# Optimization experiments

Hardware: AMD Instinct MI355X
Metric: run time of the kernel (lower is better)

## Reference

```python
import jax, jax.numpy as jnp
import numpy as np
from jax import lax

NPOINT, RADIUS, NSAMPLE, K_KEY = 64, 1.0, 32, 64

def conv1d(x, W, b):
    # 1x1 Conv1d: x [B,Cin,N], W [Cout,Cin], b [Cout] -> [B,Cout,N]
    return jnp.einsum('bcn,dc->bdn', x, W) + b[None, :, None]

def farthest_point_sample(xyz, npoint):
    # xyz [B,N,3] -> idx [B,npoint]
    B, N, _ = xyz.shape
    dist0 = jnp.full((B, N), 1e10, dtype=xyz.dtype)
    far0 = jnp.zeros((B,), dtype=jnp.int32)
    def body(carry, _):
        dist, far = carry
        centroid = jnp.take_along_axis(xyz, far[:, None, None].astype(jnp.int32), axis=1)  # [B,1,3]
        d = jnp.sum((xyz - centroid) ** 2, -1)
        dist = jnp.minimum(dist, d)
        nxt = jnp.argmax(dist, -1).astype(jnp.int32)
        return (dist, nxt), far
    _, idxs = lax.scan(body, (dist0, far0), None, length=npoint)
    return idxs.T  # [B,npoint]

def ball_query(radius, nsample, xyz, new_xyz):
    # xyz [B,N,3], new_xyz [B,S,3] -> group_idx [B,S,nsample]
    N = xyz.shape[1]
    sqr = jnp.sum((new_xyz[:, :, None, :] - xyz[:, None, :, :]) ** 2, -1)  # [B,S,N]
    gidx = jnp.where(sqr > radius ** 2, N, jnp.arange(N, dtype=jnp.int32)[None, None, :])
    gidx = jnp.sort(gidx, axis=-1)[..., :nsample]
    first = gidx[..., :1]
    gidx = jnp.where(gidx == N, first, gidx)
    return gidx

def sample_and_group(npoint, radius, nsample, xyz, points):
    # xyz [B,N,3], points [B,N,D]
    B = xyz.shape[0]
    fps_idx = farthest_point_sample(xyz, npoint)                     # [B,S]
    bidx = jnp.arange(B)[:, None]
    new_xyz = xyz[bidx, fps_idx]                                     # [B,S,3]
    gidx = ball_query(radius, nsample, xyz, new_xyz)                 # [B,S,ns]
    bidx2 = jnp.arange(B)[:, None, None]
    grouped_xyz = xyz[bidx2, gidx]                                   # [B,S,ns,3]
    grouped_xyz_norm = grouped_xyz - new_xyz[:, :, None, :]
    grouped_points = points[bidx2, gidx]                             # [B,S,ns,D]
    new_points = jnp.concatenate([grouped_xyz_norm, grouped_points], axis=-1)
    return new_xyz, new_points

def setup_inputs() -> dict:
    key = jax.random.key(0)
    ks = jax.random.split(key, 12)
    B, C, N = 8, 6, 65536
    def w(k, co, ci):
        return jax.random.normal(k, (co, ci), jnp.float32) * (1.0 / np.sqrt(ci))
    return {
        'src_pts': jax.random.normal(ks[0], (B, C, N), jnp.float32),
        'tgt_pts': jax.random.normal(ks[1], (B, C, N), jnp.float32),
        'W1': w(ks[2], 32, 6),  'b1': jnp.zeros((32,), jnp.float32),
        'W2': w(ks[3], 64, 32), 'b2': jnp.zeros((64,), jnp.float32),
        'Wa': w(ks[4], 16, 64), 'ba': jnp.zeros((16,), jnp.float32),
        'Wb': w(ks[5], 8, 16),  'bb': jnp.zeros((8,), jnp.float32),
        'Wc': w(ks[6], 1, 8),   'bc': jnp.zeros((1,), jnp.float32),
    }

def reference(src_pts, tgt_pts, W1, b1, W2, b2, Wa, ba, Wb, bb, Wc, bc):
    # feat_extraction_layer: 1x1 conv stack over points -> deep per-point features
    h = jax.nn.relu(conv1d(src_pts, W1, b1))            # [B,32,N]
    deep_feat_pts = jax.nn.relu(conv1d(h, W2, b2))      # [B,64,N]
    # weighting_layer: per-point saliency weight + top-k keypoint indices (1-D, batch-0 idiom)
    w = jax.nn.relu(conv1d(deep_feat_pts, Wa, ba))
    w = jax.nn.relu(conv1d(w, Wb, bb))
    w = jax.nn.softplus(conv1d(w, Wc, bc))              # [B,1,N]
    _, keypts_idx = lax.top_k(w[0, 0], K_KEY)           # [K]
    # irregular keypoint gather (shared index across batch, as in src_pts[:, :, idx])
    src_keypts = src_pts[:, :, keypts_idx].transpose(0, 2, 1)   # [B,K,C]
    # ball-query sample_and_group on keypoints (computed then discarded, as in original)
    _gxyz, _gpts = sample_and_group(NPOINT, RADIUS, NSAMPLE, src_keypts[:, :, :3], src_keypts[:, :, 3:])
    return src_keypts
```

## Files before the change

kernel.cpp:

```cpp
#include <hip/hip_runtime.h>
#include <stdint.h>

#define N_PTS 65536
#define NB1 32768
#define NB2 4096
#define CAND_CAP 4096
#define FCAP 1024
typedef unsigned long long u64;


__global__ __launch_bounds__(256) void zero_kernel(uint4* __restrict__ z, int n4)
{
    const int i = blockIdx.x * 256 + threadIdx.x;
    const uint4 zz = {0u, 0u, 0u, 0u};
    if (i < n4) z[i] = zz;
}

__global__ __launch_bounds__(128, 1) void score_kernel(
    const float* __restrict__ src,
    const float* __restrict__ W1, const float* __restrict__ b1,
    const float* __restrict__ W2, const float* __restrict__ b2,
    const float* __restrict__ Wa, const float* __restrict__ ba,
    const float* __restrict__ Wb, const float* __restrict__ bb,
    const float* __restrict__ Wc, const float* __restrict__ bc,
    float* __restrict__ scores, unsigned* __restrict__ hist1)
{
    __shared__ unsigned histL[NB1];
    __shared__ __align__(16) float sW1[32 * 8];
    __shared__ __align__(16) float sW2[64 * 32];
    __shared__ __align__(16) float sWaT[64 * 16];
    __shared__ __align__(16) float sWb[8 * 16];
    __shared__ float sb2[64], sba[16], sbb[8], sWc[8], sbc1[1];
    const int t = threadIdx.x;

    {
        uint4* h4 = (uint4*)histL;
        const uint4 zz = {0u, 0u, 0u, 0u};
        #pragma unroll
        for (int i = 0; i < 64; i++) h4[t + 128 * i] = zz;
    }
    for (int i = t; i < 256; i += 128) {
        const int j = i >> 3, c = i & 7;
        sW1[i] = (c < 6) ? W1[j * 6 + c] : ((c == 6) ? b1[j] : 0.f);
    }
    for (int i = t; i < 2048; i += 128) sW2[i] = W2[i];
    for (int i = t; i < 1024; i += 128) {
        const int j = i >> 4, q = i & 15;
        sWaT[i] = Wa[q * 64 + j];
    }
    if (t < 128) sWb[t] = Wb[t];
    if (t < 64)  sb2[t] = b2[t];
    if (t < 16)  sba[t] = ba[t];
    if (t < 8)   { sbb[t] = bb[t]; sWc[t] = Wc[t]; }
    if (t == 0)  sbc1[0] = bc[0];
    __syncthreads();

    const int base = blockIdx.x * 256;
    const int p[2] = { base + t, base + 128 + t };

    float x[2][6];
    #pragma unroll
    for (int c = 0; c < 6; c++) {
        x[0][c] = src[c * N_PTS + p[0]];
        x[1][c] = src[c * N_PTS + p[1]];
    }

    float h1[2][32];
    #pragma unroll
    for (int j = 0; j < 32; j++) {
        const float4 wA = *(const float4*)&sW1[j * 8];
        const float4 wB = *(const float4*)&sW1[j * 8 + 4];
        #pragma unroll
        for (int P = 0; P < 2; P++) {
            float a = wB.z;
            a = fmaf(wA.x, x[P][0], a); a = fmaf(wA.y, x[P][1], a);
            a = fmaf(wA.z, x[P][2], a); a = fmaf(wA.w, x[P][3], a);
            a = fmaf(wB.x, x[P][4], a); a = fmaf(wB.y, x[P][5], a);
            h1[P][j] = fmaxf(a, 0.f);
        }
    }

    float h3[2][16];
    #pragma unroll
    for (int q = 0; q < 16; q++) { h3[0][q] = sba[q]; h3[1][q] = sba[q]; }

    #pragma unroll 1
    for (int jb = 0; jb < 32; jb++) {
        const int j0 = 2 * jb, j1 = j0 + 1;
        const float4* r0 = (const float4*)&sW2[j0 * 32];
        const float4* r1 = (const float4*)&sW2[j1 * 32];
        const float4* wa0 = (const float4*)&sWaT[j0 * 16];
        const float4* wa1 = (const float4*)&sWaT[j1 * 16];
        float4 u[8], v[8], q0[4], q1[4];
        #pragma unroll
        for (int i = 0; i < 8; i++) u[i] = r0[i];
        #pragma unroll
        for (int i = 0; i < 8; i++) v[i] = r1[i];
        #pragma unroll
        for (int i = 0; i < 4; i++) q0[i] = wa0[i];
        #pragma unroll
        for (int i = 0; i < 4; i++) q1[i] = wa1[i];
        const float bj0 = sb2[j0], bj1 = sb2[j1];

        #pragma unroll
        for (int P = 0; P < 2; P++) {
            float a0 = 0.f, a1 = 0.f, a2 = 0.f, a3 = 0.f;
            float c0 = 0.f, c1 = 0.f, c2 = 0.f, c3 = 0.f;
            #pragma unroll
            for (int i4 = 0; i4 < 8; i4++) {
                const float h0 = h1[P][4 * i4 + 0], hh1 = h1[P][4 * i4 + 1];
                const float h2 = h1[P][4 * i4 + 2], hh3 = h1[P][4 * i4 + 3];
                a0 = fmaf(u[i4].x, h0, a0); a1 = fmaf(u[i4].y, hh1, a1);
                a2 = fmaf(u[i4].z, h2, a2); a3 = fmaf(u[i4].w, hh3, a3);
                c0 = fmaf(v[i4].x, h0, c0); c1 = fmaf(v[i4].y, hh1, c1);
                c2 = fmaf(v[i4].z, h2, c2); c3 = fmaf(v[i4].w, hh3, c3);
            }
            const float v0 = fmaxf((a0 + a1) + (a2 + a3) + bj0, 0.f);
            const float v1 = fmaxf((c0 + c1) + (c2 + c3) + bj1, 0.f);
            #pragma unroll
            for (int q4 = 0; q4 < 4; q4++) {
                float t0 = h3[P][4 * q4 + 0], t1 = h3[P][4 * q4 + 1];
                float t2 = h3[P][4 * q4 + 2], t3 = h3[P][4 * q4 + 3];
                t0 = fmaf(q0[q4].x, v0, t0); t1 = fmaf(q0[q4].y, v0, t1);
                t2 = fmaf(q0[q4].z, v0, t2); t3 = fmaf(q0[q4].w, v0, t3);
                t0 = fmaf(q1[q4].x, v1, t0); t1 = fmaf(q1[q4].y, v1, t1);
                t2 = fmaf(q1[q4].z, v1, t2); t3 = fmaf(q1[q4].w, v1, t3);
                h3[P][4 * q4 + 0] = t0; h3[P][4 * q4 + 1] = t1;
                h3[P][4 * q4 + 2] = t2; h3[P][4 * q4 + 3] = t3;
            }
        }
    }
    #pragma unroll
    for (int q = 0; q < 16; q++) {
        h3[0][q] = fmaxf(h3[0][q], 0.f);
        h3[1][q] = fmaxf(h3[1][q], 0.f);
    }

    float z[2] = { sbc1[0], sbc1[0] };
    #pragma unroll
    for (int j = 0; j < 8; j++) {
        const float4* wbr = (const float4*)&sWb[j * 16];
        const float4 w0 = wbr[0], w1 = wbr[1], w2 = wbr[2], w3 = wbr[3];
        const float bj = sbb[j], wc = sWc[j];
        #pragma unroll
        for (int P = 0; P < 2; P++) {
            float s0 = bj, s1 = 0.f, s2 = 0.f, s3 = 0.f;
            s0 = fmaf(w0.x, h3[P][0],  s0); s1 = fmaf(w0.y, h3[P][1],  s1);
            s2 = fmaf(w0.z, h3[P][2],  s2); s3 = fmaf(w0.w, h3[P][3],  s3);
            s0 = fmaf(w1.x, h3[P][4],  s0); s1 = fmaf(w1.y, h3[P][5],  s1);
            s2 = fmaf(w1.z, h3[P][6],  s2); s3 = fmaf(w1.w, h3[P][7],  s3);
            s0 = fmaf(w2.x, h3[P][8],  s0); s1 = fmaf(w2.y, h3[P][9],  s1);
            s2 = fmaf(w2.z, h3[P][10], s2); s3 = fmaf(w2.w, h3[P][11], s3);
            s0 = fmaf(w3.x, h3[P][12], s0); s1 = fmaf(w3.y, h3[P][13], s1);
            s2 = fmaf(w3.z, h3[P][14], s2); s3 = fmaf(w3.w, h3[P][15], s3);
            z[P] = fmaf(wc, fmaxf((s0 + s1) + (s2 + s3), 0.f), z[P]);
        }
    }

    #pragma unroll
    for (int P = 0; P < 2; P++) {
        const float sp = fmaxf(z[P], 0.f) + log1pf(expf(-fabsf(z[P])));
        scores[p[P]] = sp;
        atomicAdd(&histL[__float_as_uint(sp) >> 16], 1u);
    }
    __syncthreads();

    {
        const uint4* h4 = (const uint4*)histL;
        for (int i = t; i < NB1 / 4; i += 128) {
            const uint4 v = h4[i];
            if (v.x) atomicAdd(&hist1[4 * i + 0], v.x);
            if (v.y) atomicAdd(&hist1[4 * i + 1], v.y);
            if (v.z) atomicAdd(&hist1[4 * i + 2], v.z);
            if (v.w) atomicAdd(&hist1[4 * i + 3], v.w);
        }
    }
}

__global__ __launch_bounds__(256) void refine_kernel(
    const unsigned* __restrict__ hist1, const float* __restrict__ scores,
    unsigned* __restrict__ hist2, int* __restrict__ meta,
    u64* __restrict__ cand)
{
    __shared__ unsigned csum[256];
    __shared__ unsigned bsum[128];
    __shared__ int sh_c, sh_B;
    __shared__ unsigned sh_tail;
    const int t = threadIdx.x;

    {
        unsigned s = 0;
        const uint4* h4 = (const uint4*)(hist1 + t * 128);
        #pragma unroll
        for (int i = 0; i < 32; i++) {
            const uint4 v = h4[i];
            s += v.x + v.y + v.z + v.w;
        }
        csum[t] = s;
    }
    __syncthreads();
    for (int d = 1; d < 256; d <<= 1) {
        const unsigned v = (t + d < 256) ? csum[t + d] : 0u;
        __syncthreads();
        csum[t] += v;
        __syncthreads();
    }
    {
        const unsigned here = csum[t];
        const unsigned nxt = (t + 1 < 256) ? csum[t + 1] : 0u;
        if (here >= 64u && nxt < 64u) sh_c = t;
    }
    __syncthreads();
    const int cstar = sh_c;
    if (t < 128) bsum[t] = hist1[cstar * 128 + t];
    __syncthreads();
    {
        const unsigned ctail = (cstar + 1 < 256) ? csum[cstar + 1] : 0u;
        for (int d = 1; d < 128; d <<= 1) {
            unsigned v = 0u;
            if (t < 128 && t + d < 128) v = bsum[t + d];
            __syncthreads();
            if (t < 128) bsum[t] += v;
            __syncthreads();
        }
        if (t < 128) {
            const unsigned here = bsum[t] + ctail;
            const unsigned nxt = (t + 1 < 128) ? bsum[t + 1] + ctail : ctail;
            if (here >= 64u && nxt < 64u) { sh_B = cstar * 128 + t; sh_tail = nxt; }
        }
    }
    __syncthreads();
    const unsigned Bstar = (unsigned)sh_B;
    if (blockIdx.x == 0 && t == 0) { meta[0] = sh_B; meta[1] = (int)sh_tail; }

    const float4* s4 = (const float4*)scores;
    const int i = blockIdx.x * 256 + t;
    const float4 v = s4[i];
    const int n0 = 4 * i;
    #pragma unroll
    for (int k = 0; k < 4; k++) {
        const float sv = (k == 0) ? v.x : (k == 1) ? v.y : (k == 2) ? v.z : v.w;
        const unsigned b = __float_as_uint(sv);
        const unsigned hi = b >> 16;
        if (hi >= Bstar) {
            const int p = atomicAdd(&meta[2], 1);
            if (p < CAND_CAP) cand[p] = ((u64)b << 32) | (unsigned)~(n0 + k);
            if (hi == Bstar) atomicAdd(&hist2[(b & 0xFFFFu) >> 4], 1u);
        }
    }
}

__global__ __launch_bounds__(256) void final_kernel(
    const unsigned* __restrict__ hist2, const int* __restrict__ meta,
    const u64* __restrict__ cand, const float* __restrict__ src,
    float* __restrict__ out)
{
    __shared__ unsigned h2[NB2];
    __shared__ unsigned csum[256];
    __shared__ u64 keys[FCAP];
    __shared__ int idxs[64];
    __shared__ int sh_c, sh_T2, sh_cnt;
    const int t = threadIdx.x;
    const unsigned Bstar = (unsigned)meta[0];
    const unsigned tail1 = (unsigned)meta[1];

    {
        uint4* d = (uint4*)h2;
        const uint4* s = (const uint4*)hist2;
        #pragma unroll
        for (int i = 0; i < 4; i++) d[t + 256 * i] = s[t + 256 * i];
    }
    __syncthreads();

    {
        unsigned s = 0;
        #pragma unroll
        for (int i = 0; i < 16; i++) s += h2[t * 16 + i];
        csum[t] = s;
    }
    __syncthreads();
    for (int d = 1; d < 256; d <<= 1) {
        const unsigned v = (t + d < 256) ? csum[t + d] : 0u;
        __syncthreads();
        csum[t] += v;
        __syncthreads();
    }
    {
        const unsigned here = tail1 + csum[t];
        const unsigned nxt = tail1 + ((t + 1 < 256) ? csum[t + 1] : 0u);
        if (here >= 64u && nxt < 64u) sh_c = t;
    }
    __syncthreads();
    {
        const int c2 = sh_c;
        if (t == 0) {
            unsigned acc = tail1 + ((c2 + 1 < 256) ? csum[c2 + 1] : 0u);
            int T2 = c2 * 16;
            for (int b = c2 * 16 + 15; b >= c2 * 16; b--) {
                acc += h2[b];
                if (acc >= 64u) { T2 = b; break; }
            }
            sh_T2 = T2;
            sh_cnt = 0;
        }
    }
    __syncthreads();
    const unsigned T2 = (unsigned)sh_T2;

    int count = meta[2];
    if (count > CAND_CAP) count = CAND_CAP;
    for (int i = t; i < count; i += 256) {
        const u64 key = cand[i];
        const unsigned b = (unsigned)(key >> 32);
        const unsigned hi = b >> 16;
        if (hi > Bstar || ((b & 0xFFFFu) >> 4) >= T2) {
            const int p = atomicAdd(&sh_cnt, 1);
            if (p < FCAP) keys[p] = key;
        }
    }
    __syncthreads();

    int fcnt = sh_cnt;
    if (fcnt > FCAP) fcnt = FCAP;
    for (int i = t; i < fcnt; i += 256) {
        const u64 me = keys[i];
        int r = 0;
        for (int j = 0; j < fcnt; j++) r += (keys[j] > me);
        if (r < 64) idxs[r] = (int)~(unsigned)(me & 0xFFFFFFFFu);
    }
    __syncthreads();

    for (int e = t; e < 3072; e += 256) {
        const int b  = e / 384;
        const int rr = e % 384;
        const int kk = rr / 6;
        const int c  = rr % 6;
        out[e] = src[(b * 6 + c) * N_PTS + idxs[kk]];
    }
}

extern "C" void kernel_launch(void* const* d_in, const int* in_sizes, int n_in,
                              void* d_out, int out_size, void* d_ws, size_t ws_size,
                              hipStream_t stream)
{
    const float* src = (const float*)d_in[0];
    const float* W1 = (const float*)d_in[2];
    const float* b1 = (const float*)d_in[3];
    const float* W2 = (const float*)d_in[4];
    const float* b2 = (const float*)d_in[5];
    const float* Wa = (const float*)d_in[6];
    const float* ba = (const float*)d_in[7];
    const float* Wb = (const float*)d_in[8];
    const float* bb = (const float*)d_in[9];
    const float* Wc = (const float*)d_in[10];
    const float* bc = (const float*)d_in[11];

    char* ws = (char*)d_ws;
    float*    scores = (float*)ws;
    unsigned* hist1  = (unsigned*)(ws + 256 * 1024);
    unsigned* hist2  = (unsigned*)(ws + 384 * 1024);
    int*      meta   = (int*)(ws + 400 * 1024);
    u64*      cand   = (u64*)(ws + 408 * 1024);
    float*    out    = (float*)d_out;

    const int n4 = (NB1 + NB2 + 16) / 4;
    zero_kernel<<<(n4 + 255) / 256, 256, 0, stream>>>((uint4*)hist1, n4);
    score_kernel<<<256, 128, 0, stream>>>(src, W1, b1, W2, b2, Wa, ba,
                                          Wb, bb, Wc, bc, scores, hist1);
    refine_kernel<<<64, 256, 0, stream>>>(hist1, scores, hist2, meta, cand);
    final_kernel<<<1, 256, 0, stream>>>(hist2, meta, cand, src, out);
}
```

Baseline: 148.6 us.

## Fuse final selection into refine via last-block pattern and enlarge score blocks

The final single-block kernel is merged into refine_kernel: each block increments a completion counter after its candidate pass, and only the last-arriving block runs the final top-k selection and gather. This removes one kernel launch and its serialization gap. score_kernel also moves from 256 blocks of 128 threads to 64 blocks of 512 threads, so fewer blocks each zero and flush the 32K-bin shared histogram, cutting global atomic traffic. The cost is only 64 blocks on a large GPU for the MLP work, plus threadfence ordering and the counter in meta[3], which must be zeroed before each call.

```diff
diff --git a/kernel.cpp b/kernel.cpp
--- a/kernel.cpp
+++ b/kernel.cpp
@@ -16,7 +16,7 @@
     if (i < n4) z[i] = zz;
 }
 
-__global__ __launch_bounds__(128, 1) void score_kernel(
+__global__ __launch_bounds__(512, 1) void score_kernel(
     const float* __restrict__ src,
     const float* __restrict__ W1, const float* __restrict__ b1,
     const float* __restrict__ W2, const float* __restrict__ b2,
@@ -37,14 +37,14 @@
         uint4* h4 = (uint4*)histL;
         const uint4 zz = {0u, 0u, 0u, 0u};
         #pragma unroll
-        for (int i = 0; i < 64; i++) h4[t + 128 * i] = zz;
-    }
-    for (int i = t; i < 256; i += 128) {
-        const int j = i >> 3, c = i & 7;
-        sW1[i] = (c < 6) ? W1[j * 6 + c] : ((c == 6) ? b1[j] : 0.f);
-    }
-    for (int i = t; i < 2048; i += 128) sW2[i] = W2[i];
-    for (int i = t; i < 1024; i += 128) {
+        for (int i = 0; i < 16; i++) h4[t + 512 * i] = zz;
+    }
+    if (t < 256) {
+        const int j = t >> 3, c = t & 7;
+        sW1[t] = (c < 6) ? W1[j * 6 + c] : ((c == 6) ? b1[j] : 0.f);
+    }
+    for (int i = t; i < 2048; i += 512) sW2[i] = W2[i];
+    for (int i = t; i < 1024; i += 512) {
         const int j = i >> 4, q = i & 15;
         sWaT[i] = Wa[q * 64 + j];
     }
@@ -55,8 +55,8 @@
     if (t == 0)  sbc1[0] = bc[0];
     __syncthreads();
 
-    const int base = blockIdx.x * 256;
-    const int p[2] = { base + t, base + 128 + t };
+    const int base = blockIdx.x * 1024;
+    const int p[2] = { base + t, base + 512 + t };
 
     float x[2][6];
     #pragma unroll
@@ -167,7 +167,7 @@
 
     {
         const uint4* h4 = (const uint4*)histL;
-        for (int i = t; i < NB1 / 4; i += 128) {
+        for (int i = t; i < NB1 / 4; i += 512) {
             const uint4 v = h4[i];
             if (v.x) atomicAdd(&hist1[4 * i + 0], v.x);
             if (v.y) atomicAdd(&hist1[4 * i + 1], v.y);
@@ -180,12 +180,16 @@
 __global__ __launch_bounds__(256) void refine_kernel(
     const unsigned* __restrict__ hist1, const float* __restrict__ scores,
     unsigned* __restrict__ hist2, int* __restrict__ meta,
-    u64* __restrict__ cand)
+    u64* __restrict__ cand, const float* __restrict__ src,
+    float* __restrict__ out)
 {
     __shared__ unsigned csum[256];
     __shared__ unsigned bsum[128];
-    __shared__ int sh_c, sh_B;
-    __shared__ unsigned sh_tail;
+    __shared__ unsigned h2[NB2];
+    __shared__ u64 keys[FCAP];
+    __shared__ int idxs[64];
+    __shared__ int sh_c, sh_B, sh_T2, sh_cnt;
+    __shared__ unsigned sh_tail, sh_rank;
     const int t = threadIdx.x;
 
     {
@@ -231,38 +235,32 @@
     }
     __syncthreads();
     const unsigned Bstar = (unsigned)sh_B;
-    if (blockIdx.x == 0 && t == 0) { meta[0] = sh_B; meta[1] = (int)sh_tail; }
-
-    const float4* s4 = (const float4*)scores;
-    const int i = blockIdx.x * 256 + t;
-    const float4 v = s4[i];
-    const int n0 = 4 * i;
-    #pragma unroll
-    for (int k = 0; k < 4; k++) {
-        const float sv = (k == 0) ? v.x : (k == 1) ? v.y : (k == 2) ? v.z : v.w;
-        const unsigned b = __float_as_uint(sv);
-        const unsigned hi = b >> 16;
-        if (hi >= Bstar) {
-            const int p = atomicAdd(&meta[2], 1);
-            if (p < CAND_CAP) cand[p] = ((u64)b << 32) | (unsigned)~(n0 + k);
-            if (hi == Bstar) atomicAdd(&hist2[(b & 0xFFFFu) >> 4], 1u);
-        }
-    }
-}
-
-__global__ __launch_bounds__(256) void final_kernel(
-    const unsigned* __restrict__ hist2, const int* __restrict__ meta,
-    const u64* __restrict__ cand, const float* __restrict__ src,
-    float* __restrict__ out)
-{
-    __shared__ unsigned h2[NB2];
-    __shared__ unsigned csum[256];
-    __shared__ u64 keys[FCAP];
-    __shared__ int idxs[64];
-    __shared__ int sh_c, sh_T2, sh_cnt;
-    const int t = threadIdx.x;
-    const unsigned Bstar = (unsigned)meta[0];
-    const unsigned tail1 = (unsigned)meta[1];
+    const unsigned tail1 = sh_tail;
+
+    {
+        const float4* s4 = (const float4*)scores;
+        const int i = blockIdx.x * 256 + t;
+        const float4 v = s4[i];
+        const int n0 = 4 * i;
+        #pragma unroll
+        for (int k = 0; k < 4; k++) {
+            const float sv = (k == 0) ? v.x : (k == 1) ? v.y : (k == 2) ? v.z : v.w;
+            const unsigned b = __float_as_uint(sv);
+            const unsigned hi = b >> 16;
+            if (hi >= Bstar) {
+                const int p = atomicAdd(&meta[2], 1);
+                if (p < CAND_CAP) cand[p] = ((u64)b << 32) | (unsigned)~(n0 + k);
+                if (hi == Bstar) atomicAdd(&hist2[(b & 0xFFFFu) >> 4], 1u);
+            }
+        }
+    }
+
+    __syncthreads();
+    __threadfence();
+    if (t == 0) sh_rank = atomicAdd((unsigned*)&meta[3], 1u);
+    __syncthreads();
+    if (sh_rank != 63u) return;
+    __threadfence();
 
     {
         uint4* d = (uint4*)h2;
@@ -365,8 +363,8 @@
 
     const int n4 = (NB1 + NB2 + 16) / 4;
     zero_kernel<<<(n4 + 255) / 256, 256, 0, stream>>>((uint4*)hist1, n4);
-    score_kernel<<<256, 128, 0, stream>>>(src, W1, b1, W2, b2, Wa, ba,
-                                          Wb, bb, Wc, bc, scores, hist1);
-    refine_kernel<<<64, 256, 0, stream>>>(hist1, scores, hist2, meta, cand);
-    final_kernel<<<1, 256, 0, stream>>>(hist2, meta, cand, src, out);
+    score_kernel<<<64, 512, 0, stream>>>(src, W1, b1, W2, b2, Wa, ba,
+                                         Wb, bb, Wc, bc, scores, hist1);
+    refine_kernel<<<64, 256, 0, stream>>>(hist1, scores, hist2, meta, cand,
+                                          src, out);
 }
```

Result: faster. 144.0 us (-3.0%).
